# Kernel optimization log

Hardware: AMD Instinct MI355X
Metric: run time of the kernel (lower is better)

Reference implementation:

```python
import jax, jax.numpy as jnp
import numpy as np

K = 8                      # neighbors per node (module default)
MUL0, MUL1, MUL2 = 64, 32, 16   # multiplicities of 0e, 1o, 2e
D = MUL0 + 3 * MUL1 + 5 * MUL2  # 240 = irreps dim


def _w3j_112():
    """Wigner-3j-like coupling 1 x 1 -> 2 (real basis), Frobenius norm 1 like e3nn."""
    M = np.zeros((5, 3, 3), dtype=np.float32)
    s = 1.0 / np.sqrt(2.0)
    M[0, 0, 1] = M[0, 1, 0] = s          # xy
    M[1, 0, 2] = M[1, 2, 0] = s          # xz
    M[2, 1, 2] = M[2, 2, 1] = s          # yz
    M[3, 0, 0] = s; M[3, 1, 1] = -s      # x^2 - y^2
    t = 1.0 / np.sqrt(6.0)
    M[4, 0, 0] = -t; M[4, 1, 1] = -t; M[4, 2, 2] = 2 * t  # 2z^2 - x^2 - y^2
    return jnp.asarray(np.transpose(M, (1, 2, 0)) / np.sqrt(5.0))  # [3,3,5]

C112 = _w3j_112()                         # coupling for 1o x 1o -> 2e
C211 = jnp.transpose(C112, (2, 0, 1))     # cyclic permutation: 2e x 1o -> 1o


def _knn_edges(coords, k):
    """Per-batch kNN graph; returns flat (senders, receivers) into [B*N] node ids."""
    B, N, _ = coords.shape
    d2 = jnp.sum((coords[:, :, None, :] - coords[:, None, :, :]) ** 2, -1)  # [B,N,N]
    d2 = d2 + jnp.eye(N, dtype=coords.dtype) * 1e9  # exclude self
    _, nbr = jax.lax.top_k(-d2, k)                  # [B,N,k] neighbor indices
    offs = (jnp.arange(B) * N)[:, None, None]
    senders = (nbr + offs).reshape(-1)
    receivers = jnp.broadcast_to(jnp.arange(N)[None, :, None] + offs, (B, N, k)).reshape(-1)
    return senders, receivers


def setup_inputs() -> dict:
    key = jax.random.key(0)
    ks = jax.random.split(key, 9)
    B, N = 4, 4096
    return {
        "node_feats": jax.random.normal(ks[0], (B, N, D), jnp.float32),
        "coords": jax.random.normal(ks[1], (B, N, 3), jnp.float32) * 10.0,
        "W1": jax.random.normal(ks[2], (MUL0, MUL1), jnp.float32),  # 0e x 1o -> 1o
        "W2": jax.random.normal(ks[3], (MUL1, MUL0), jnp.float32),  # 1o x 1o -> 0e
        "W3": jax.random.normal(ks[4], (MUL1, MUL2), jnp.float32),  # 1o x 1o -> 2e
        "W4": jax.random.normal(ks[5], (MUL2, MUL1), jnp.float32),  # 2e x 1o -> 1o
        "L0": jax.random.normal(ks[6], (MUL0, MUL0), jnp.float32),
        "L1": jax.random.normal(ks[7], (MUL1, MUL1), jnp.float32),
        "L2": jax.random.normal(ks[8], (MUL2, MUL2), jnp.float32),
    }


def reference(node_feats, coords, W1, W2, W3, W4, L0, L1, L2):
    B, N, _ = node_feats.shape
    senders, receivers = _knn_edges(coords, K)
    cf = coords.reshape(-1, 3)
    ev = cf[senders] - cf[receivers]              # [E,3] edge vectors (1x1o)
    xj = node_feats.reshape(-1, D)[senders]       # per-edge gather of sender feats
    x0 = xj[:, :MUL0]                             # [E,64]   0e
    x1 = xj[:, MUL0:MUL0 + 3 * MUL1].reshape(-1, MUL1, 3)  # [E,32,3] 1o
    x2 = xj[:, MUL0 + 3 * MUL1:].reshape(-1, MUL2, 5)      # [E,16,5] 2e

    # FullyConnectedTensorProduct (component irrep norm, 'element' path norm)
    # fan_in to 1o output: MUL0 + MUL2 = 80; to 0e: 32; to 2e: 32.
    m1 = jnp.sqrt(1.0 / (MUL0 + MUL2)) * jnp.einsum('eu,ek,uw->ewk', x0, ev, W1)
    m1 = m1 + jnp.sqrt(3.0 / (MUL0 + MUL2)) * jnp.einsum('eua,ajk,ej,uw->ewk', x2, C211, ev, W4)
    m0 = jnp.sqrt(1.0 / (3.0 * MUL1)) * jnp.einsum('eui,ei,uw->ew', x1, ev, W2)
    m2 = jnp.sqrt(5.0 / MUL1) * jnp.einsum('eui,ej,ijk,uw->ewk', x1, ev, C112, W3)
    msg = jnp.concatenate([m0, m1.reshape(-1, 3 * MUL1), m2.reshape(-1, 5 * MUL2)], axis=-1)

    # scatter-add aggregation at receivers
    agg = jax.ops.segment_sum(msg, receivers, num_segments=B * N)  # [B*N, D]

    # equivariant Linear: per-irrep multiplicity mixing, fan_in-normalized
    y0 = (agg[:, :MUL0] @ L0) / jnp.sqrt(float(MUL0))
    y1 = jnp.einsum('nuk,uw->nwk', agg[:, MUL0:MUL0 + 3 * MUL1].reshape(-1, MUL1, 3), L1) / jnp.sqrt(float(MUL1))
    y2 = jnp.einsum('nuk,uw->nwk', agg[:, MUL0 + 3 * MUL1:].reshape(-1, MUL2, 5), L2) / jnp.sqrt(float(MUL2))
    out = jnp.concatenate([y0, y1.reshape(-1, 3 * MUL1), y2.reshape(-1, 5 * MUL2)], axis=-1)
    return out.reshape(B, N, D)
```

## Files before the change

### kernel.cpp

```cpp
#include <hip/hip_runtime.h>

#define NN   4096
#define KNBR 8
#define DF   240
#define NSUB 16
#define QPB  64

#define OFF_PD   49152
#define OFF_PI   86016
#define OFF_THR  104448
#define OFF_NBR  104704
#define OFF_WF   0
#define OFF_SEV  20480
#define OFF_SNB  26624
#define OFF_ACC  28672
#define SMEM_SZ  106752

__device__ __forceinline__ void insD9(float v, float t[9]) {
#pragma unroll
  for (int k = 8; k >= 1; k--)
    t[k] = __builtin_amdgcn_fmed3f(t[k - 1], t[k], v);
  t[0] = fminf(t[0], v);
}

__device__ __forceinline__ void insertDI(float d2, int j, float bd[KNBR],
                                         int bi[KNBR]) {
#pragma unroll
  for (int k = KNBR - 1; k >= 1; k--) {
    bool mk  = d2 < bd[k];
    bool mk1 = d2 < bd[k - 1];
    bd[k] = mk ? (mk1 ? bd[k - 1] : d2) : bd[k];
    bi[k] = mk ? (mk1 ? bi[k - 1] : j) : bi[k];
  }
  bool m0 = d2 < bd[0];
  bd[0] = m0 ? d2 : bd[0];
  bi[0] = m0 ? j : bi[0];
}

__global__ __launch_bounds__(1024, 4) void fused_all(
    const float* __restrict__ feats, const float* __restrict__ coords,
    const float* __restrict__ W1, const float* __restrict__ W2,
    const float* __restrict__ W3, const float* __restrict__ W4,
    const float* __restrict__ L0, const float* __restrict__ L1,
    const float* __restrict__ L2, float* __restrict__ out) {
  __shared__ __align__(16) char smem[SMEM_SZ];

  const int blk = blockIdx.x;
  const int b = blk >> 6;
  const int chunk = blk & 63;
  const int qi  = threadIdx.x & 63;
  const int sub = threadIdx.x >> 6;
  const int iq  = chunk * 64 + qi;
  const float* cb = coords + (size_t)b * NN * 3;
  const float4* cb4 = (const float4*)cb;

  float4* cnd = (float4*)smem;
  float* pdB = (float*)(smem + OFF_PD);
  unsigned short* piB = (unsigned short*)(smem + OFF_PI);
  float* thrS = (float*)(smem + OFF_THR);
  int* nbrL = (int*)(smem + OFF_NBR);

  {
    int t = threadIdx.x;
    cnd[t]        = cb4[t];
    cnd[1024 + t] = cb4[1024 + t];
    cnd[2048 + t] = cb4[2048 + t];
  }
  const float qx = cb[iq * 3 + 0], qy = cb[iq * 3 + 1], qz = cb[iq * 3 + 2];
  __syncthreads();

  const int j0 = sub * 256;

  float t0v = 3.0e38f, t1v = 3.0e38f;
#pragma unroll 4
  for (int g = 0; g < 64; ++g) {
    int f = 3 * (sub * 64 + g);
    float4 f0 = cnd[f + 0];
    float4 f1 = cnd[f + 1];
    float4 f2 = cnd[f + 2];
    float xs[4] = {f0.x, f0.w, f1.z, f2.y};
    float ys[4] = {f0.y, f1.x, f1.w, f2.z};
    float zs[4] = {f0.z, f1.y, f2.x, f2.w};
#pragma unroll
    for (int c = 0; c < 4; ++c) {
      float dx = xs[c] - qx, dy = ys[c] - qy, dz = zs[c] - qz;
      float d2 = dx * dx + dy * dy + dz * dz;
      t1v = __builtin_amdgcn_fmed3f(t0v, t1v, d2);
      t0v = fminf(t0v, d2);
    }
  }
  pdB[(sub * 64 + qi) * 9 + 0] = t0v;
  pdB[(sub * 64 + qi) * 9 + 1] = t1v;
  __syncthreads();

  if (threadIdx.x < 64) {
    const int q = threadIdx.x;
    float md[9];
#pragma unroll
    for (int k = 0; k < 9; k++) md[k] = 3.0e38f;
    for (int s = 0; s < NSUB; s++) {
      insD9(pdB[(s * 64 + q) * 9 + 0], md);
      insD9(pdB[(s * 64 + q) * 9 + 1], md);
    }
    thrS[q] = md[8];
  }
  __syncthreads();

  const float tq = thrS[qi];
  float bd[KNBR];
  int bi[KNBR];
#pragma unroll
  for (int k = 0; k < KNBR; k++) { bd[k] = 3.0e38f; bi[k] = 0; }
#pragma unroll 2
  for (int g = 0; g < 64; ++g) {
    int base = j0 + 4 * g;
    int f = 3 * (sub * 64 + g);
    float4 f0 = cnd[f + 0];
    float4 f1 = cnd[f + 1];
    float4 f2 = cnd[f + 2];
    float xs[4] = {f0.x, f0.w, f1.z, f2.y};
    float ys[4] = {f0.y, f1.x, f1.w, f2.z};
    float zs[4] = {f0.z, f1.y, f2.x, f2.w};
    float d2s[4];
#pragma unroll
    for (int c = 0; c < 4; ++c) {
      float dx = xs[c] - qx, dy = ys[c] - qy, dz = zs[c] - qz;
      float d2 = dx * dx + dy * dy + dz * dz;
      d2s[c] = (base + c == iq) ? 3.0e38f : d2;
    }
    float m4 = fminf(fminf(d2s[0], d2s[1]), fminf(d2s[2], d2s[3]));
    if (m4 <= tq) {
#pragma unroll
      for (int c = 0; c < 4; ++c)
        if (d2s[c] <= tq) insertDI(d2s[c], base + c, bd, bi);
    }
  }
#pragma unroll
  for (int k = 0; k < KNBR; k++) {
    pdB[(sub * 64 + qi) * 9 + k] = bd[k];
    piB[(sub * 64 + qi) * 9 + k] = (unsigned short)bi[k];
  }
  __syncthreads();

  if (threadIdx.x < 64) {
    const int q = threadIdx.x;
    float md[KNBR];
    int mi[KNBR];
#pragma unroll
    for (int k = 0; k < KNBR; k++) { md[k] = 3.0e38f; mi[k] = 0; }
    for (int s = 0; s < NSUB; s++) {
#pragma unroll
      for (int k = 0; k < KNBR; k++) {
        float vd = pdB[(s * 64 + q) * 9 + k];
        if (vd < md[KNBR - 1]) insertDI(vd, (int)piB[(s * 64 + q) * 9 + k],
                                        md, mi);
      }
    }
#pragma unroll
    for (int k = 0; k < KNBR; k++) nbrL[q * KNBR + k] = mi[k];
  }
  __syncthreads();

  float* WfL  = (float*)(smem + OFF_WF);
  float* sevL = (float*)(smem + OFF_SEV);
  int*   snbL = (int*)(smem + OFF_SNB);
  float* accL = (float*)(smem + OFF_ACC);

  {
    const float sA = 0.012757759076995719f;
    const float sB = 0.019764235376052370f;
    const float sC = 0.034232659844072875f;
    const float sD = 0.098821176880261850f;
#pragma unroll
    for (int i = 0; i < 5; i++) {
      int idx = threadIdx.x + 1024 * i;
      if (idx < 2048) {
        int u2 = idx >> 6, c = idx & 63;
        float a = 0.f;
#pragma unroll 8
        for (int m = 0; m < 64; m++) a += W2[u2 * 64 + m] * L0[m * 64 + c];
        WfL[idx] = sA * a;
      } else if (idx < 4096) {
        int t = idx - 2048;
        int u2 = t >> 5, c = t & 31;
        float a = 0.f;
#pragma unroll 8
        for (int m = 0; m < 32; m++) a += W1[u2 * 32 + m] * L1[m * 32 + c];
        WfL[idx] = sB * a;
      } else if (idx < 4608) {
        int t = idx - 4096;
        int u2 = t >> 5, c = t & 31;
        float a = 0.f;
#pragma unroll 8
        for (int m = 0; m < 32; m++) a += W4[u2 * 32 + m] * L1[m * 32 + c];
        WfL[idx] = sC * a;
      } else {
        int t = idx - 4608;
        int u2 = t >> 4, c = t & 15;
        float a = 0.f;
#pragma unroll 8
        for (int m = 0; m < 16; m++) a += W3[u2 * 16 + m] * L2[m * 16 + c];
        WfL[idx] = sD * a;
      }
    }
  }
  if (threadIdx.x < 512) {
    int t = threadIdx.x;
    int nl = t >> 3, e = t & 7;
    int jj = nbrL[nl * KNBR + e];
    int iqn = chunk * 64 + nl;
    snbL[t] = b * NN + jj;
    sevL[3 * t + 0] = cb[jj * 3 + 0] - cb[iqn * 3 + 0];
    sevL[3 * t + 1] = cb[jj * 3 + 1] - cb[iqn * 3 + 1];
    sevL[3 * t + 2] = cb[jj * 3 + 2] - cb[iqn * 3 + 2];
  }
  __syncthreads();

  const float S_ = 0.31622776601683794f;
  const float T_ = 0.18257418583505536f;
  const int w = threadIdx.x >> 6;
  const int u = threadIdx.x & 63;
  float* A = accL + w * 432;

  for (int i2 = 0; i2 < 4; i2++) {
    const int nl = w * 4 + i2;
    const int node = blk * 64 + nl;

    float z0x = 0.f, z0y = 0.f, z0z = 0.f;
    float s1 = 0.f, p0 = 0.f, p1 = 0.f, p2 = 0.f, p3 = 0.f, p4 = 0.f;
    float q0 = 0.f, q1 = 0.f, q2 = 0.f;

#pragma unroll
    for (int h = 0; h < 2; h++) {
      const float* fr[4];
      float xv[4], av0[4], av1[4], av2[4];
      float bv0[4], bv1[4], bv2[4], bv3[4], bv4[4];
#pragma unroll
      for (int i = 0; i < 4; i++) {
        fr[i] = feats + (size_t)snbL[nl * KNBR + 4 * h + i] * DF;
        xv[i] = fr[i][u];
      }
      if (u < 32) {
#pragma unroll
        for (int i = 0; i < 4; i++) {
          av0[i] = fr[i][64 + 3 * u];
          av1[i] = fr[i][65 + 3 * u];
          av2[i] = fr[i][66 + 3 * u];
        }
        if (u < 16) {
#pragma unroll
          for (int i = 0; i < 4; i++) {
            bv0[i] = fr[i][160 + 5 * u];
            bv1[i] = fr[i][161 + 5 * u];
            bv2[i] = fr[i][162 + 5 * u];
            bv3[i] = fr[i][163 + 5 * u];
            bv4[i] = fr[i][164 + 5 * u];
          }
        }
      }
#pragma unroll
      for (int i = 0; i < 4; i++) {
        const int e = 4 * h + i;
        float X = sevL[(nl * KNBR + e) * 3 + 0];
        float Y = sevL[(nl * KNBR + e) * 3 + 1];
        float Z = sevL[(nl * KNBR + e) * 3 + 2];
        float sxv = S_ * X, syv = S_ * Y, szv = S_ * Z;
        float txv = T_ * X, tyv = T_ * Y, t2z = 2.f * T_ * Z;
        z0x += xv[i] * X;
        z0y += xv[i] * Y;
        z0z += xv[i] * Z;
        if (u < 32) {
          s1 += av0[i] * X + av1[i] * Y + av2[i] * Z;
          p0 += av0[i] * syv + av1[i] * sxv;
          p1 += av0[i] * szv + av2[i] * sxv;
          p2 += av1[i] * szv + av2[i] * syv;
          p3 += av0[i] * sxv - av1[i] * syv;
          p4 += av2[i] * t2z - av0[i] * txv - av1[i] * tyv;
          if (u < 16) {
            q0 += bv0[i] * syv + bv1[i] * szv + bv3[i] * sxv - bv4[i] * txv;
            q1 += bv0[i] * sxv + bv2[i] * szv - bv3[i] * syv - bv4[i] * tyv;
            q2 += bv1[i] * sxv + bv2[i] * syv + bv4[i] * t2z;
          }
        }
      }
    }

    A[32 + 3 * u + 0] = z0x;
    A[32 + 3 * u + 1] = z0y;
    A[32 + 3 * u + 2] = z0z;
    if (u < 32) {
      A[u] = s1;
      float* pp = A + 224 + 5 * u;
      pp[0] = p0; pp[1] = p1; pp[2] = p2; pp[3] = p3; pp[4] = p4;
    }
    if (u < 16) {
      float* qq = A + 384 + 3 * u;
      qq[0] = q0; qq[1] = q1; qq[2] = q2;
    }
    asm volatile("s_waitcnt lgkmcnt(0)" ::: "memory");

    const float* WA = WfL;
    const float* WB = WfL + 2048;
    const float* WC = WfL + 4096;
    const float* WD = WfL + 4608;
    float* orow = out + (size_t)node * DF;

    {
      float a = 0.f;
#pragma unroll
      for (int m = 0; m < 32; m++) a += A[m] * WA[m * 64 + u];
      orow[u] = a;
    }
#pragma unroll
    for (int m0 = 0; m0 < 96; m0 += 64) {
      int m = m0 + u;
      if (m < 96) {
        int w1 = m / 3, k = m - w1 * 3;
        float a = 0.f;
#pragma unroll
        for (int t = 0; t < 64; t++) a += A[32 + 3 * t + k] * WB[t * 32 + w1];
#pragma unroll
        for (int t = 0; t < 16; t++) a += A[384 + 3 * t + k] * WC[t * 32 + w1];
        orow[64 + m] = a;
      }
    }
#pragma unroll
    for (int m0 = 0; m0 < 80; m0 += 64) {
      int m = m0 + u;
      if (m < 80) {
        int w2 = m / 5, k = m - w2 * 5;
        float a = 0.f;
#pragma unroll
        for (int t = 0; t < 32; t++) a += A[224 + 5 * t + k] * WD[t * 16 + w2];
        orow[160 + m] = a;
      }
    }
    asm volatile("s_waitcnt lgkmcnt(0)" ::: "memory");
  }
}

extern "C" void kernel_launch(void* const* d_in, const int* in_sizes, int n_in,
                              void* d_out, int out_size, void* d_ws,
                              size_t ws_size, hipStream_t stream) {
  const float* feats  = (const float*)d_in[0];
  const float* coords = (const float*)d_in[1];
  const float* W1 = (const float*)d_in[2];
  const float* W2 = (const float*)d_in[3];
  const float* W3 = (const float*)d_in[4];
  const float* W4 = (const float*)d_in[5];
  const float* L0 = (const float*)d_in[6];
  const float* L1 = (const float*)d_in[7];
  const float* L2 = (const float*)d_in[8];
  float* out = (float*)d_out;
  (void)d_ws; (void)ws_size;

  fused_all<<<256, 1024, 0, stream>>>(feats, coords, W1, W2, W3, W4, L0, L1,
                                      L2, out);
}
```

Measured before the change: 190.2 us.

## Software-pipeline neighbor feature gathers and interleave batches across blocks

```diff
diff --git a/kernel.cpp b/kernel.cpp
--- a/kernel.cpp
+++ b/kernel.cpp
@@ -37,6 +37,66 @@
   bi[0] = m0 ? j : bi[0];
 }
 
+#define CH_DECL(P)                                                  \
+  const float* P##fr[4];                                            \
+  float P##xv[4], P##av0[4], P##av1[4], P##av2[4],                  \
+        P##bv0[4], P##bv1[4], P##bv2[4], P##bv3[4], P##bv4[4];
+
+#define CH_LOAD(P, NL, H)                                           \
+  do {                                                              \
+    _Pragma("unroll") for (int i = 0; i < 4; i++) {                 \
+      P##fr[i] =                                                    \
+          feats + (size_t)snbL[(NL) * KNBR + 4 * (H) + i] * DF;     \
+      P##xv[i] = P##fr[i][u];                                       \
+    }                                                               \
+    if (u < 32) {                                                   \
+      _Pragma("unroll") for (int i = 0; i < 4; i++) {               \
+        P##av0[i] = P##fr[i][64 + 3 * u];                           \
+        P##av1[i] = P##fr[i][65 + 3 * u];                           \
+        P##av2[i] = P##fr[i][66 + 3 * u];                           \
+      }                                                             \
+      if (u < 16) {                                                 \
+        _Pragma("unroll") for (int i = 0; i < 4; i++) {             \
+          P##bv0[i] = P##fr[i][160 + 5 * u];                        \
+          P##bv1[i] = P##fr[i][161 + 5 * u];                        \
+          P##bv2[i] = P##fr[i][162 + 5 * u];                        \
+          P##bv3[i] = P##fr[i][163 + 5 * u];                        \
+          P##bv4[i] = P##fr[i][164 + 5 * u];                        \
+        }                                                           \
+      }                                                             \
+    }                                                               \
+  } while (0)
+
+#define CH_CONS(P, NL, H)                                           \
+  do {                                                              \
+    _Pragma("unroll") for (int i = 0; i < 4; i++) {                 \
+      const int e = 4 * (H) + i;                                    \
+      float X = sevL[((NL) * KNBR + e) * 3 + 0];                    \
+      float Y = sevL[((NL) * KNBR + e) * 3 + 1];                    \
+      float Z = sevL[((NL) * KNBR + e) * 3 + 2];                    \
+      float sxv = S_ * X, syv = S_ * Y, szv = S_ * Z;               \
+      float txv = T_ * X, tyv = T_ * Y, t2z = 2.f * T_ * Z;         \
+      z0x += P##xv[i] * X;                                          \
+      z0y += P##xv[i] * Y;                                          \
+      z0z += P##xv[i] * Z;                                          \
+      if (u < 32) {                                                 \
+        s1 += P##av0[i] * X + P##av1[i] * Y + P##av2[i] * Z;        \
+        p0 += P##av0[i] * syv + P##av1[i] * sxv;                    \
+        p1 += P##av0[i] * szv + P##av2[i] * sxv;                    \
+        p2 += P##av1[i] * szv + P##av2[i] * syv;                    \
+        p3 += P##av0[i] * sxv - P##av1[i] * syv;                    \
+        p4 += P##av2[i] * t2z - P##av0[i] * txv - P##av1[i] * tyv;  \
+        if (u < 16) {                                               \
+          q0 += P##bv0[i] * syv + P##bv1[i] * szv +                 \
+                P##bv3[i] * sxv - P##bv4[i] * txv;                  \
+          q1 += P##bv0[i] * sxv + P##bv2[i] * szv -                 \
+                P##bv3[i] * syv - P##bv4[i] * tyv;                  \
+          q2 += P##bv1[i] * sxv + P##bv2[i] * syv + P##bv4[i] * t2z;\
+        }                                                           \
+      }                                                             \
+    }                                                               \
+  } while (0)
+
 __global__ __launch_bounds__(1024, 4) void fused_all(
     const float* __restrict__ feats, const float* __restrict__ coords,
     const float* __restrict__ W1, const float* __restrict__ W2,
@@ -46,8 +106,8 @@
   __shared__ __align__(16) char smem[SMEM_SZ];
 
   const int blk = blockIdx.x;
-  const int b = blk >> 6;
-  const int chunk = blk & 63;
+  const int b = blk & 3;
+  const int chunk = blk >> 2;
   const int qi  = threadIdx.x & 63;
   const int sub = threadIdx.x >> 6;
   const int iq  = chunk * 64 + qi;
@@ -72,7 +132,7 @@
   const int j0 = sub * 256;
 
   float t0v = 3.0e38f, t1v = 3.0e38f;
-#pragma unroll 4
+#pragma unroll 8
   for (int g = 0; g < 64; ++g) {
     int f = 3 * (sub * 64 + g);
     float4 f0 = cnd[f + 0];
@@ -222,68 +282,22 @@
   const int u = threadIdx.x & 63;
   float* A = accL + w * 432;
 
+  CH_DECL(cA_)
+  CH_DECL(cB_)
+  CH_LOAD(cA_, w * 4, 0);
+
   for (int i2 = 0; i2 < 4; i2++) {
     const int nl = w * 4 + i2;
-    const int node = blk * 64 + nl;
+    const int node = b * NN + chunk * 64 + nl;
 
     float z0x = 0.f, z0y = 0.f, z0z = 0.f;
     float s1 = 0.f, p0 = 0.f, p1 = 0.f, p2 = 0.f, p3 = 0.f, p4 = 0.f;
     float q0 = 0.f, q1 = 0.f, q2 = 0.f;
 
-#pragma unroll
-    for (int h = 0; h < 2; h++) {
-      const float* fr[4];
-      float xv[4], av0[4], av1[4], av2[4];
-      float bv0[4], bv1[4], bv2[4], bv3[4], bv4[4];
-#pragma unroll
-      for (int i = 0; i < 4; i++) {
-        fr[i] = feats + (size_t)snbL[nl * KNBR + 4 * h + i] * DF;
-        xv[i] = fr[i][u];
-      }
-      if (u < 32) {
-#pragma unroll
-        for (int i = 0; i < 4; i++) {
-          av0[i] = fr[i][64 + 3 * u];
-          av1[i] = fr[i][65 + 3 * u];
-          av2[i] = fr[i][66 + 3 * u];
-        }
-        if (u < 16) {
-#pragma unroll
-          for (int i = 0; i < 4; i++) {
-            bv0[i] = fr[i][160 + 5 * u];
-            bv1[i] = fr[i][161 + 5 * u];
-            bv2[i] = fr[i][162 + 5 * u];
-            bv3[i] = fr[i][163 + 5 * u];
-            bv4[i] = fr[i][164 + 5 * u];
-          }
-        }
-      }
-#pragma unroll
-      for (int i = 0; i < 4; i++) {
-        const int e = 4 * h + i;
-        float X = sevL[(nl * KNBR + e) * 3 + 0];
-        float Y = sevL[(nl * KNBR + e) * 3 + 1];
-        float Z = sevL[(nl * KNBR + e) * 3 + 2];
-        float sxv = S_ * X, syv = S_ * Y, szv = S_ * Z;
-        float txv = T_ * X, tyv = T_ * Y, t2z = 2.f * T_ * Z;
-        z0x += xv[i] * X;
-        z0y += xv[i] * Y;
-        z0z += xv[i] * Z;
-        if (u < 32) {
-          s1 += av0[i] * X + av1[i] * Y + av2[i] * Z;
-          p0 += av0[i] * syv + av1[i] * sxv;
-          p1 += av0[i] * szv + av2[i] * sxv;
-          p2 += av1[i] * szv + av2[i] * syv;
-          p3 += av0[i] * sxv - av1[i] * syv;
-          p4 += av2[i] * t2z - av0[i] * txv - av1[i] * tyv;
-          if (u < 16) {
-            q0 += bv0[i] * syv + bv1[i] * szv + bv3[i] * sxv - bv4[i] * txv;
-            q1 += bv0[i] * sxv + bv2[i] * szv - bv3[i] * syv - bv4[i] * tyv;
-            q2 += bv1[i] * sxv + bv2[i] * syv + bv4[i] * t2z;
-          }
-        }
-      }
-    }
+    CH_LOAD(cB_, nl, 1);
+    CH_CONS(cA_, nl, 0);
+    if (i2 < 3) CH_LOAD(cA_, nl + 1, 0);
+    CH_CONS(cB_, nl, 1);
 
     A[32 + 3 * u + 0] = z0x;
     A[32 + 3 * u + 1] = z0y;
```

Measured after the change: 230.0 us. +20.9%, slower.
